# Kernel optimization log

Measured on AMD Instinct MI355X. Metric: run time of the kernel, lower is better.

Reference implementation:

```python
import jax, jax.numpy as jnp
import numpy as np

EPS = 1e-6

def safe_softmax(x, axis=-1):
    x_max = jnp.max(x, axis=axis, keepdims=True)
    x_exp = jnp.exp(x - x_max)
    return x_exp / (jnp.sum(x_exp, axis=axis, keepdims=True) + EPS)

def setup_inputs() -> dict:
    key = jax.random.key(0)
    ks = jax.random.split(key, 8)
    B, S, D = 16, 2048, 1024
    scale = 1.0 / np.sqrt(D)
    x = jax.random.normal(ks[0], (B, S, D), dtype=jnp.float32)
    y = jax.random.normal(ks[1], (B, S, D), dtype=jnp.float32)
    Wq = jax.random.normal(ks[2], (D, D), dtype=jnp.float32) * scale
    bq = jnp.zeros((D,), dtype=jnp.float32)
    Wk = jax.random.normal(ks[3], (D, D), dtype=jnp.float32) * scale
    bk = jnp.zeros((D,), dtype=jnp.float32)
    Wv = jax.random.normal(ks[4], (D, D), dtype=jnp.float32) * scale
    bv = jnp.zeros((D,), dtype=jnp.float32)
    return {"x": x, "y": y, "Wq": Wq, "bq": bq, "Wk": Wk, "bk": bk, "Wv": Wv, "bv": bv}

def reference(x, y, Wq, bq, Wk, bk, Wv, bv):
    # Q/K/V projections: [B, S, D]
    Q = jnp.einsum('bsd,df->bsf', x, Wq) + bq
    K = jnp.einsum('bsd,df->bsf', y, Wk) + bk
    V = jnp.einsum('bsd,df->bsf', y, Wv) + bv
    D = K.shape[-1]
    # single-head attention over full [B, Sq, Skv] score matrix
    logits = jnp.einsum('bqd,bkd->bqk', Q, K) / jnp.sqrt(jnp.float32(D))
    attn = safe_softmax(logits, axis=-1)
    out = jnp.einsum('bqk,bkd->bqd', attn, V)
    return out + x
```

## Files before the change

kernel.cpp:

```cpp
#include <hip/hip_runtime.h>
#include <hip/hip_bf16.h>

typedef __attribute__((ext_vector_type(8))) short bf16x8;
typedef __attribute__((ext_vector_type(4))) float f32x4;

__device__ __forceinline__ float bf2f(short u) {
  union { unsigned int u; float f; } c;
  c.u = ((unsigned int)(unsigned short)u) << 16;
  return c.f;
}
__device__ __forceinline__ short f2bf(float f) {
  union { float f; unsigned int u; } c; c.f = f;
  unsigned int r = (c.u + 0x7fffu + ((c.u >> 16) & 1u)) >> 16;
  return (short)(unsigned short)r;
}

__device__ __forceinline__ void gload16(const void* g, void* l) {
  __builtin_amdgcn_global_load_lds(
      (const __attribute__((address_space(1))) unsigned int*)g,
      (__attribute__((address_space(3))) unsigned int*)l, 16, 0, 0);
}

__global__ __launch_bounds__(256) void cvt_k(const float* __restrict__ in,
                                             short* __restrict__ out, int n4) {
  int i = blockIdx.x * blockDim.x + threadIdx.x;
  const int stride = gridDim.x * blockDim.x;
  for (; i < n4; i += stride) {
    float4 v = ((const float4*)in)[i];
    short4 o;
    o.x = f2bf(v.x); o.y = f2bf(v.y); o.z = f2bf(v.z); o.w = f2bf(v.w);
    ((short4*)out)[i] = o;
  }
}

__global__ __launch_bounds__(256) void cvtT_k(const float* __restrict__ W,
                                              short* __restrict__ Wt) {
  __shared__ float tile[32][33];
  const int n0 = blockIdx.x * 32, k0 = blockIdx.y * 32;
  const int tr = threadIdx.x >> 5;
  const int tc = threadIdx.x & 31;
#pragma unroll
  for (int p = 0; p < 4; ++p)
    tile[p * 8 + tr][tc] = W[(long long)(k0 + p * 8 + tr) * 1024 + n0 + tc];
  __syncthreads();
#pragma unroll
  for (int p = 0; p < 4; ++p)
    Wt[(long long)(n0 + p * 8 + tr) * 1024 + k0 + tc] = f2bf(tile[tc][p * 8 + tr]);
}


#define STG(sp, ld8, dOff) do { \
  gload16((sp), Ls + (dOff)); \
  gload16((const char*)(sp) + (ld8), Ls + (dOff) + 512); } while (0)

#define RD_A(QM) do { \
  _Pragma("unroll") \
  for (int mi = 0; mi < 4; ++mi) { \
    aR[mi][0] = *(const bf16x8*)(Ls + bufS + (QM)*8192 + arow + mi*1024 + aO0); \
    aR[mi][1] = *(const bf16x8*)(Ls + bufS + (QM)*8192 + arow + mi*1024 + aO1); \
  } } while (0)

#define RD_B(DST, QN) do { \
  _Pragma("unroll") \
  for (int ni = 0; ni < 2; ++ni) { \
    DST[ni][0] = *(const bf16x8*)(Ls + bufS + 16384 + (QN)*8192 + brow + ni*1024 + aO0); \
    DST[ni][1] = *(const bf16x8*)(Ls + bufS + 16384 + (QN)*8192 + brow + ni*1024 + aO1); \
  } } while (0)

#define SYNCIN do { \
  __builtin_amdgcn_sched_barrier(0); \
  __builtin_amdgcn_s_barrier(); \
  asm volatile("s_waitcnt lgkmcnt(0)" ::: "memory"); \
  __builtin_amdgcn_sched_barrier(0); \
  __builtin_amdgcn_s_setprio(1); } while (0)

#define SYNCOUT do { \
  __builtin_amdgcn_s_setprio(0); \
  __builtin_amdgcn_s_barrier(); } while (0)

#define MF16(ACCQ, BB) do { \
  _Pragma("unroll") \
  for (int mi = 0; mi < 4; ++mi) { \
    _Pragma("unroll") \
    for (int ni = 0; ni < 2; ++ni) { \
      ACCQ[mi][ni] = __builtin_amdgcn_mfma_f32_16x16x32_bf16(aR[mi][0], BB[ni][0], ACCQ[mi][ni], 0, 0, 0); \
      ACCQ[mi][ni] = __builtin_amdgcn_mfma_f32_16x16x32_bf16(aR[mi][1], BB[ni][1], ACCQ[mi][ni], 0, 0, 0); \
    } \
  } } while (0)

template<int EPI>
__global__ __launch_bounds__(512) void gemm8_k(
    const short* __restrict__ A, const short* __restrict__ Bt,
    void* __restrict__ Cv, const float* __restrict__ X,
    int K, int lda, int ldb, int ldc,
    long long sA, long long sB, long long sC, long long sX, float scale) {
  __shared__ __align__(16) short Ls[65536];

  const int lane = threadIdx.x & 63;
  const int w = threadIdx.x >> 6;
  const int wm = w >> 2, wn = w & 3;
  const int w1k = w * 1024;
  const int l15 = lane & 15;
  const int g4 = lane >> 4;
  const int p8 = lane & 7;
  const int r8 = lane >> 3;
  const int aO0 = (g4 ^ p8) << 3;
  const int aO1 = ((4 + g4) ^ p8) << 3;
  const int arow = (wm * 64 + l15) * 64;
  const int brow = (wn * 32 + l15) * 64;

  const int gx = gridDim.x, gy = gridDim.y;
  const int nwg = gx * gy * gridDim.z;
  int lid = blockIdx.x + gx * (blockIdx.y + gy * blockIdx.z);
  lid = (lid & 7) * (nwg >> 3) + (lid >> 3);
  const int bx = lid % gx;
  const int rem = lid / gx;
  const int by = rem % gy;
  const int bz = rem / gy;

  const int n0 = bx * 256;
  const int m0 = by * 256;
  const int nt = K >> 6;

  const long long ldaB = 2LL * lda, ldbB = 2LL * ldb;
  const long long ldaB8 = 8 * ldaB, ldbB8 = 8 * ldbB;
  const long long hOffA = 128 * ldaB, hOffB = 128 * ldbB;

  const char* pA = (const char*)(A + (long long)bz * sA)
      + (long long)(m0 + w * 16 + r8) * ldaB + ((p8 ^ r8) << 4);
  const char* pB = (const char*)(Bt + (long long)bz * sB)
      + (long long)(n0 + w * 16 + r8) * ldbB + ((p8 ^ r8) << 4);

  f32x4 acc[2][2][4][2] = {};
  bf16x8 aR[4][2], bR0[2][2], bR1[2][2];

  STG(pA,          ldaB8, 0 + w1k);
  STG(pA + hOffA,  ldaB8, 8192 + w1k);
  STG(pB,          ldbB8, 16384 + w1k);
  STG(pB + hOffB,  ldbB8, 24576 + w1k);
  if (nt > 1) {
    STG(pA + 128, ldaB8, 32768 + w1k);
    STG(pB + 128, ldbB8, 49152 + w1k);
    asm volatile("s_waitcnt vmcnt(4)" ::: "memory");
  } else {
    asm volatile("s_waitcnt vmcnt(0)" ::: "memory");
  }
  __builtin_amdgcn_s_barrier();

  for (int t = 0; t < nt; ++t) {
    const int bufS = (t & 1) << 15;
    const int obufS = bufS ^ 32768;
    const bool st1 = (t + 1 < nt), st2 = (t + 2 < nt);

    RD_A(0); RD_B(bR0, 0);
    if (st1) { STG(pA + 128 + hOffA, ldaB8, obufS + 8192 + w1k);
               STG(pB + 128 + hOffB, ldbB8, obufS + 24576 + w1k); }
    SYNCIN;
    MF16(acc[0][0], bR0);
    SYNCOUT;

    RD_B(bR1, 1);
    if (st2) STG(pA + 256, ldaB8, bufS + w1k);
    SYNCIN;
    MF16(acc[0][1], bR1);
    SYNCOUT;

    RD_A(1);
    if (st2) STG(pB + 256, ldbB8, bufS + 16384 + w1k);
    SYNCIN;
    MF16(acc[1][1], bR1);
    MF16(acc[1][0], bR0);
    __builtin_amdgcn_s_setprio(0);
    if (st2)      asm volatile("s_waitcnt vmcnt(4)" ::: "memory");
    else if (st1) asm volatile("s_waitcnt vmcnt(0)" ::: "memory");
    __builtin_amdgcn_s_barrier();

    pA += 128; pB += 128;
  }

  const int rB = g4 * 4;
  if (EPI == 0) {
    short* C = (short*)Cv + (long long)bz * sC;
#pragma unroll
    for (int qn = 0; qn < 2; ++qn)
#pragma unroll
      for (int ni = 0; ni < 2; ++ni) {
        const int col = n0 + qn * 128 + wn * 32 + ni * 16 + l15;
        const float bv = X[col];
#pragma unroll
        for (int qm = 0; qm < 2; ++qm)
#pragma unroll
          for (int mi = 0; mi < 4; ++mi)
#pragma unroll
            for (int r = 0; r < 4; ++r) {
              const int row = m0 + qm * 128 + wm * 64 + mi * 16 + rB + r;
              C[(long long)row * ldc + col] = f2bf(acc[qm][qn][mi][ni][r] + bv);
            }
      }
  } else if (EPI == 1) {
    short* C = (short*)Cv + (long long)bz * sC;
#pragma unroll
    for (int qn = 0; qn < 2; ++qn)
#pragma unroll
      for (int ni = 0; ni < 2; ++ni) {
        const int col = n0 + qn * 128 + wn * 32 + ni * 16 + l15;
#pragma unroll
        for (int qm = 0; qm < 2; ++qm)
#pragma unroll
          for (int mi = 0; mi < 4; ++mi)
#pragma unroll
            for (int r = 0; r < 4; ++r) {
              const int row = m0 + qm * 128 + wm * 64 + mi * 16 + rB + r;
              C[(long long)row * ldc + col] = f2bf(acc[qm][qn][mi][ni][r] * scale);
            }
      }
  } else if (EPI == 2) {
    float* C = (float*)Cv + (long long)bz * sC;
    const float* Xb = X + (long long)bz * sX;
#pragma unroll
    for (int qn = 0; qn < 2; ++qn)
#pragma unroll
      for (int ni = 0; ni < 2; ++ni) {
        const int col = n0 + qn * 128 + wn * 32 + ni * 16 + l15;
#pragma unroll
        for (int qm = 0; qm < 2; ++qm)
#pragma unroll
          for (int mi = 0; mi < 4; ++mi)
#pragma unroll
            for (int r = 0; r < 4; ++r) {
              const int row = m0 + qm * 128 + wm * 64 + mi * 16 + rB + r;
              const long long idx = (long long)row * ldc + col;
              C[idx] = acc[qm][qn][mi][ni][r] + Xb[idx];
            }
      }
  } else {
    short* C = (short*)Cv;
#pragma unroll
    for (int qn = 0; qn < 2; ++qn)
#pragma unroll
      for (int ni = 0; ni < 2; ++ni) {
        const int col = n0 + qn * 128 + wn * 32 + ni * 16 + l15;
        const int bb = col >> 11;
        const int s = col & 2047;
#pragma unroll
        for (int qm = 0; qm < 2; ++qm)
#pragma unroll
          for (int mi = 0; mi < 4; ++mi)
#pragma unroll
            for (int r = 0; r < 4; ++r) {
              const int row = m0 + qm * 128 + wm * 64 + mi * 16 + rB + r;
              C[(long long)bb * 2097152 + (long long)row * 2048 + s] =
                  f2bf(acc[qm][qn][mi][ni][r] + X[row]);
            }
      }
  }
}

__global__ __launch_bounds__(256) void softmax_k(short* __restrict__ P) {
  __shared__ float redm[4];
  __shared__ float reds[4];
  const long long row = blockIdx.x;
  short* p = P + row * 2048;
  const int t = threadIdx.x;
  const int w = t >> 6, lane = t & 63;
  bf16x8 v = *(const bf16x8*)(p + t * 8);
  float f[8];
  float mx = -3.0e38f;
#pragma unroll
  for (int j = 0; j < 8; ++j) { f[j] = bf2f(v[j]); mx = fmaxf(mx, f[j]); }
#pragma unroll
  for (int o = 32; o > 0; o >>= 1) mx = fmaxf(mx, __shfl_xor(mx, o));
  if (lane == 0) redm[w] = mx;
  __syncthreads();
  mx = fmaxf(fmaxf(redm[0], redm[1]), fmaxf(redm[2], redm[3]));
  float s = 0.f;
#pragma unroll
  for (int j = 0; j < 8; ++j) { f[j] = __expf(f[j] - mx); s += f[j]; }
#pragma unroll
  for (int o = 32; o > 0; o >>= 1) s += __shfl_xor(s, o);
  if (lane == 0) reds[w] = s;
  __syncthreads();
  s = reds[0] + reds[1] + reds[2] + reds[3];
  const float inv = 1.0f / (s + 1e-6f);
  bf16x8 o8;
#pragma unroll
  for (int j = 0; j < 8; ++j) o8[j] = f2bf(f[j] * inv);
  *(bf16x8*)(p + t * 8) = o8;
}

extern "C" void kernel_launch(void* const* d_in, const int* in_sizes, int n_in,
                              void* d_out, int out_size, void* d_ws, size_t ws_size,
                              hipStream_t stream) {
  const float* x  = (const float*)d_in[0];
  const float* y  = (const float*)d_in[1];
  const float* Wq = (const float*)d_in[2];
  const float* bq = (const float*)d_in[3];
  const float* Wk = (const float*)d_in[4];
  const float* bk = (const float*)d_in[5];
  const float* Wv = (const float*)d_in[6];
  const float* bv = (const float*)d_in[7];
  float* out = (float*)d_out;

  const long long SD  = 2048LL * 1024;
  const long long BSD = 16LL * SD;
  const long long SS  = 2048LL * 2048;

  char* ws = (char*)d_ws;
  short* xb  = (short*)ws;
  short* yb  = xb + BSD;
  short* Sl  = (short*)ws;
  short* Qb  = (short*)(ws + 134217728);
  short* Kb  = Qb + BSD;
  short* Vt  = Kb + BSD;
  short* Wqt = Vt + BSD;
  short* Wkt = Wqt + 1024 * 1024;
  short* Wvt = Wkt + 1024 * 1024;

  cvt_k<<<2048, 256, 0, stream>>>(x, xb, (int)(BSD / 4));
  cvt_k<<<2048, 256, 0, stream>>>(y, yb, (int)(BSD / 4));

  cvtT_k<<<dim3(32, 32), 256, 0, stream>>>(Wq, Wqt);
  cvtT_k<<<dim3(32, 32), 256, 0, stream>>>(Wk, Wkt);
  cvtT_k<<<dim3(32, 32), 256, 0, stream>>>(Wv, Wvt);

  gemm8_k<0><<<dim3(4, 128, 1), 512, 0, stream>>>(
      xb, Wqt, Qb, bq, 1024, 1024, 1024, 1024, 0, 0, 0, 0, 1.f);
  gemm8_k<0><<<dim3(4, 128, 1), 512, 0, stream>>>(
      yb, Wkt, Kb, bk, 1024, 1024, 1024, 1024, 0, 0, 0, 0, 1.f);
  gemm8_k<3><<<dim3(128, 4, 1), 512, 0, stream>>>(
      Wvt, yb, Vt, bv, 1024, 1024, 1024, 0, 0, 0, 0, 0, 1.f);

  gemm8_k<1><<<dim3(8, 8, 16), 512, 0, stream>>>(
      Qb, Kb, Sl, nullptr, 1024, 1024, 1024, 2048, SD, SD, SS, 0, 0.03125f);

  softmax_k<<<32768, 256, 0, stream>>>(Sl);

  gemm8_k<2><<<dim3(4, 8, 16), 512, 0, stream>>>(
      Sl, Vt, out, x, 2048, 2048, 2048, 1024, SS, SD, SD, SD, 1.f);

  (void)in_sizes; (void)n_in; (void)out_size; (void)ws_size;
}
```

Before: 728.3 us.

## Unroll GEMM main loop by two with a restructured double-buffer prefetch schedule

The bf16 GEMM main loop is unrolled by two so each half uses a fixed LDS buffer offset instead of a computed one. Global-to-LDS prefetches of the next K-tile are now issued as whole tiles, with four staged quarter-loads spread across the four MFMA phases, and the wait is vmcnt(8) instead of the earlier split scheme. The aim is to overlap loads more evenly with compute and cut per-iteration address and branch overhead. It assumes nt is even and at least 2, and it adds a fourth barrier phase per K-step, which could cost some synchronisation time.

```diff
diff --git a/kernel.cpp b/kernel.cpp
--- a/kernel.cpp
+++ b/kernel.cpp
@@ -53,18 +53,18 @@
   gload16((sp), Ls + (dOff)); \
   gload16((const char*)(sp) + (ld8), Ls + (dOff) + 512); } while (0)
 
-#define RD_A(QM) do { \
+#define RD_A(BUF, QM) do { \
   _Pragma("unroll") \
   for (int mi = 0; mi < 4; ++mi) { \
-    aR[mi][0] = *(const bf16x8*)(Ls + bufS + (QM)*8192 + arow + mi*1024 + aO0); \
-    aR[mi][1] = *(const bf16x8*)(Ls + bufS + (QM)*8192 + arow + mi*1024 + aO1); \
+    aR[mi][0] = *(const bf16x8*)(Ls + (BUF) + (QM)*8192 + arow + mi*1024 + aO0); \
+    aR[mi][1] = *(const bf16x8*)(Ls + (BUF) + (QM)*8192 + arow + mi*1024 + aO1); \
   } } while (0)
 
-#define RD_B(DST, QN) do { \
+#define RD_B(DST, BUF, QN) do { \
   _Pragma("unroll") \
   for (int ni = 0; ni < 2; ++ni) { \
-    DST[ni][0] = *(const bf16x8*)(Ls + bufS + 16384 + (QN)*8192 + brow + ni*1024 + aO0); \
-    DST[ni][1] = *(const bf16x8*)(Ls + bufS + 16384 + (QN)*8192 + brow + ni*1024 + aO1); \
+    DST[ni][0] = *(const bf16x8*)(Ls + (BUF) + 16384 + (QN)*8192 + brow + ni*1024 + aO0); \
+    DST[ni][1] = *(const bf16x8*)(Ls + (BUF) + 16384 + (QN)*8192 + brow + ni*1024 + aO1); \
   } } while (0)
 
 #define SYNCIN do { \
@@ -121,6 +121,7 @@
   const int n0 = bx * 256;
   const int m0 = by * 256;
   const int nt = K >> 6;
+  const int nit = nt >> 1;
 
   const long long ldaB = 2LL * lda, ldbB = 2LL * ldb;
   const long long ldaB8 = 8 * ldaB, ldbB8 = 8 * ldbB;
@@ -134,48 +135,52 @@
   f32x4 acc[2][2][4][2] = {};
   bf16x8 aR[4][2], bR0[2][2], bR1[2][2];
 
-  STG(pA,          ldaB8, 0 + w1k);
-  STG(pA + hOffA,  ldaB8, 8192 + w1k);
-  STG(pB,          ldbB8, 16384 + w1k);
-  STG(pB + hOffB,  ldbB8, 24576 + w1k);
-  if (nt > 1) {
-    STG(pA + 128, ldaB8, 32768 + w1k);
-    STG(pB + 128, ldbB8, 49152 + w1k);
-    asm volatile("s_waitcnt vmcnt(4)" ::: "memory");
-  } else {
-    asm volatile("s_waitcnt vmcnt(0)" ::: "memory");
-  }
+  STG(pA,                 ldaB8, 0 + w1k);
+  STG(pA + hOffA,         ldaB8, 8192 + w1k);
+  STG(pB,                 ldbB8, 16384 + w1k);
+  STG(pB + hOffB,         ldbB8, 24576 + w1k);
+  STG(pA + 128,           ldaB8, 32768 + w1k);
+  STG(pA + 128 + hOffA,   ldaB8, 40960 + w1k);
+  STG(pB + 128,           ldbB8, 49152 + w1k);
+  STG(pB + 128 + hOffB,   ldbB8, 57344 + w1k);
+  asm volatile("s_waitcnt vmcnt(8)" ::: "memory");
   __builtin_amdgcn_s_barrier();
 
-  for (int t = 0; t < nt; ++t) {
-    const int bufS = (t & 1) << 15;
-    const int obufS = bufS ^ 32768;
-    const bool st1 = (t + 1 < nt), st2 = (t + 2 < nt);
-
-    RD_A(0); RD_B(bR0, 0);
-    if (st1) { STG(pA + 128 + hOffA, ldaB8, obufS + 8192 + w1k);
-               STG(pB + 128 + hOffB, ldbB8, obufS + 24576 + w1k); }
-    SYNCIN;
-    MF16(acc[0][0], bR0);
-    SYNCOUT;
-
-    RD_B(bR1, 1);
-    if (st2) STG(pA + 256, ldaB8, bufS + w1k);
-    SYNCIN;
-    MF16(acc[0][1], bR1);
-    SYNCOUT;
-
-    RD_A(1);
-    if (st2) STG(pB + 256, ldbB8, bufS + 16384 + w1k);
-    SYNCIN;
-    MF16(acc[1][1], bR1);
-    MF16(acc[1][0], bR0);
+  for (int j = 0; j < nit; ++j) {
+    const bool st = (j + 1 < nit);
+
+    RD_A(0, 0); RD_B(bR0, 0, 0);
+    SYNCIN; MF16(acc[0][0], bR0); SYNCOUT;
+    RD_B(bR1, 0, 1);
+    if (st) { STG(pA + 256, ldaB8, 0 + w1k);
+              STG(pB + 256, ldbB8, 16384 + w1k); }
+    SYNCIN; MF16(acc[0][1], bR1); SYNCOUT;
+    RD_A(0, 1);
+    if (st) STG(pB + 256 + hOffB, ldbB8, 24576 + w1k);
+    SYNCIN; MF16(acc[1][1], bR1); SYNCOUT;
+    if (st) STG(pA + 256 + hOffA, ldaB8, 8192 + w1k);
+    SYNCIN; MF16(acc[1][0], bR0);
     __builtin_amdgcn_s_setprio(0);
-    if (st2)      asm volatile("s_waitcnt vmcnt(4)" ::: "memory");
-    else if (st1) asm volatile("s_waitcnt vmcnt(0)" ::: "memory");
+    if (st) asm volatile("s_waitcnt vmcnt(8)" ::: "memory");
+    else    asm volatile("s_waitcnt vmcnt(0)" ::: "memory");
     __builtin_amdgcn_s_barrier();
 
-    pA += 128; pB += 128;
+    RD_A(32768, 0); RD_B(bR0, 32768, 0);
+    SYNCIN; MF16(acc[0][0], bR0); SYNCOUT;
+    RD_B(bR1, 32768, 1);
+    if (st) { STG(pA + 384, ldaB8, 32768 + w1k);
+              STG(pB + 384, ldbB8, 49152 + w1k); }
+    SYNCIN; MF16(acc[0][1], bR1); SYNCOUT;
+    RD_A(32768, 1);
+    if (st) STG(pB + 384 + hOffB, ldbB8, 57344 + w1k);
+    SYNCIN; MF16(acc[1][1], bR1); SYNCOUT;
+    if (st) STG(pA + 384 + hOffA, ldaB8, 40960 + w1k);
+    SYNCIN; MF16(acc[1][0], bR0);
+    __builtin_amdgcn_s_setprio(0);
+    if (st) asm volatile("s_waitcnt vmcnt(8)" ::: "memory");
+    __builtin_amdgcn_s_barrier();
+
+    pA += 256; pB += 256;
   }
 
   const int rB = g4 * 4;
```

New measurement: 736.9 us. No clear change (+1.2%).
